# Optimization experiments

Measured on AMD Instinct MI355X. Metric: run time of the kernel, lower is better.

## Reference

```python
import jax, jax.numpy as jnp
import numpy as np

N_NODES = 100000

def _gcn_layer(h, src, dst, norm, W, b, n_nodes):
    # GCNConv: x @ W, then symmetric-normalized scatter-add over edges (incl. self-loops)
    h = h @ W                                  # [N, F_out]
    msg = h[src] * norm[:, None]               # [E_tot, F_out]
    out = jax.ops.segment_sum(msg, dst, num_segments=n_nodes)
    return out + b


def setup_inputs() -> dict:
    key = jax.random.key(0)
    k1, k2, k3, k4 = jax.random.split(key, 4)
    N, E, F_in, H, C = N_NODES, 3200000, 128, 16, 16
    x = jax.random.normal(k1, (N, F_in), dtype=jnp.float32)
    edge_index = jax.random.randint(k2, (2, E), 0, N, dtype=jnp.int64)
    W1 = jax.random.normal(k3, (F_in, H), dtype=jnp.float32) * (1.0 / np.sqrt(F_in))
    b1 = jnp.zeros((H,), dtype=jnp.float32)
    W2 = jax.random.normal(k4, (H, C), dtype=jnp.float32) * (1.0 / np.sqrt(H))
    b2 = jnp.zeros((C,), dtype=jnp.float32)
    return {"x": x, "edge_index": edge_index, "W1": W1, "b1": b1, "W2": W2, "b2": b2}


def reference(x, edge_index, W1, b1, W2, b2):
    N = x.shape[0]
    loops = jnp.arange(N, dtype=edge_index.dtype)
    src = jnp.concatenate([edge_index[0], loops])  # messages flow src -> dst (PyG convention)
    dst = jnp.concatenate([edge_index[1], loops])
    # symmetric normalization: deg^{-1/2}[src] * deg^{-1/2}[dst], deg counted on dst w/ self-loops
    deg = jnp.zeros((N,), dtype=x.dtype).at[dst].add(1.0)
    dinv = jax.lax.rsqrt(jnp.where(deg > 0, deg, 1.0))
    norm = dinv[src] * dinv[dst]                   # [E_tot]

    h = _gcn_layer(x, src, dst, norm, W1, b1, N)
    h = jax.nn.relu(h)
    # F.dropout(training=self.training): eval mode -> identity (deterministic reference)
    h = _gcn_layer(h, src, dst, norm, W2, b2, N)
    return jax.nn.log_softmax(h, axis=1)
```

## Files before the change

### kernel.cpp

```cpp
#include <hip/hip_runtime.h>
#include <hip/hip_bf16.h>
#include <math.h>


#define F_IN 128
#define H 16
#define NPB 128
#define MAX_NB 800
#define NBLK 256
#define BINT 1024
#define SMAX 4864
#define PFD 6

typedef __hip_bfloat16 bf16;

__device__ __forceinline__ float bflo(unsigned v) { return __uint_as_float(v << 16); }
__device__ __forceinline__ float bfhi(unsigned v) { return __uint_as_float(v & 0xffff0000u); }

__device__ __forceinline__ int swz(int p) { return (p & 7) * 32 + (p >> 3); }

__global__ void bin1_kernel(const int* __restrict__ src, const int* __restrict__ dst,
                            int* __restrict__ gcursor, unsigned* __restrict__ packed,
                            int E, int NB) {
    __shared__ int h[MAX_NB];
    __shared__ int pos[MAX_NB];
    int b = swz(blockIdx.x);
    long long e0 = (long long)E * b / NBLK;
    long long e1 = (long long)E * (b + 1) / NBLK;
    for (int i = threadIdx.x; i < NB; i += BINT) h[i] = 0;
    __syncthreads();
    for (long long e = e0 + threadIdx.x; e < e1; e += BINT)
        atomicAdd(&h[dst[e] >> 7], 1);
    __syncthreads();
    for (int i = threadIdx.x; i < NB; i += BINT) {
        int c = h[i];
        pos[i] = (c > 0) ? atomicAdd(&gcursor[i], c) : 0;
    }
    __syncthreads();
    for (long long e = e0 + threadIdx.x; e < e1; e += BINT) {
        int d = dst[e];
        int bk = d >> 7;
        int loc = atomicAdd(&pos[bk], 1);
        if (loc < SMAX)
            packed[(size_t)bk * SMAX + loc] = (unsigned)src[e] | ((unsigned)(d & 127) << 17);
    }
}

__global__ void bucketscan_kernel(const int* __restrict__ gcursor, int* __restrict__ base, int NB) {
    __shared__ int s[1024];
    int t = threadIdx.x;
    int v = 0;
    if (t < NB) { v = gcursor[t]; if (v > SMAX) v = SMAX; }
    s[t] = v;
    __syncthreads();
    for (int off = 1; off < 1024; off <<= 1) {
        int w = (t >= off) ? s[t - off] : 0;
        __syncthreads();
        s[t] += w;
        __syncthreads();
    }
    if (t < NB) base[t] = s[t] - v;
    if (t == NB - 1) base[NB] = s[t];
}

__global__ void sortcsr_kernel(const unsigned* __restrict__ packed, const int* __restrict__ gcursor,
                               const int* __restrict__ base, unsigned* __restrict__ sorted,
                               int* __restrict__ rowptr, float* __restrict__ dinv, int N) {
    __shared__ unsigned ssort[SMAX];
    __shared__ int cnt[NPB], offs[NPB], cur[NPB];
    int b = blockIdx.x;
    int rp = b * SMAX;
    int len = gcursor[b];
    if (len > SMAX) len = SMAX;
    int e0 = base[b];
    int T = blockDim.x;

    for (int i = threadIdx.x; i < NPB; i += T) cnt[i] = 0;
    __syncthreads();
    for (int i = threadIdx.x; i < len; i += T)
        atomicAdd(&cnt[packed[rp + i] >> 17], 1);
    __syncthreads();
    if (threadIdx.x < NPB) offs[threadIdx.x] = cnt[threadIdx.x];
    __syncthreads();
    for (int off = 1; off < NPB; off <<= 1) {
        int v = 0;
        if (threadIdx.x < NPB && threadIdx.x >= off) v = offs[threadIdx.x - off];
        __syncthreads();
        if (threadIdx.x < NPB) offs[threadIdx.x] += v;
        __syncthreads();
    }
    if (threadIdx.x < NPB) {
        int ex = offs[threadIdx.x] - cnt[threadIdx.x];
        cur[threadIdx.x] = ex;
        int node = b * NPB + threadIdx.x;
        if (node < N) {
            rowptr[node] = e0 + ex;
            dinv[node] = rsqrtf(1.0f + (float)cnt[threadIdx.x]);
        }
    }
    __syncthreads();
    for (int i = threadIdx.x; i < len; i += T) {
        unsigned p = packed[rp + i];
        int pos = atomicAdd(&cur[p >> 17], 1);
        ssort[pos] = p;
    }
    __syncthreads();
    for (int i = threadIdx.x; i < len; i += T) sorted[e0 + i] = ssort[i];
    if (b == 0 && threadIdx.x == 0) rowptr[N] = base[gridDim.x];
}

#define XPAD 132
__global__ void xw1_kernel(const float* __restrict__ x, const float* __restrict__ W1,
                           const float* __restrict__ dinv, bf16* __restrict__ u, int n) {
    __shared__ float sW1[F_IN * H];
    __shared__ float sx[16 * XPAD];
    for (int t = threadIdx.x; t < F_IN * H; t += blockDim.x) sW1[t] = W1[t];

    int basei = blockIdx.x * 16;
    for (int idx = threadIdx.x; idx < 512; idx += 256) {
        int r = idx >> 5;
        int kk = (idx & 31) << 2;
        int row = basei + r;
        float4 v = make_float4(0.f, 0.f, 0.f, 0.f);
        if (row < n) v = *(const float4*)(x + (size_t)row * F_IN + kk);
        *(float4*)(sx + r * XPAD + kk) = v;
    }
    __syncthreads();

    int r = threadIdx.x >> 4;
    int j = threadIdx.x & 15;
    int row = basei + r;
    if (row >= n) return;

    const float* xr = sx + r * XPAD;
    float acc = 0.0f;
#pragma unroll 16
    for (int k = 0; k < F_IN; k++) acc += xr[k] * sW1[k * H + j];
    u[(size_t)row * H + j] = __float2bfloat16(dinv[row] * acc);
}

#define GATHER_TILE(UVPTR)                                                      \
    int lane = threadIdx.x & 63;                                                \
    int wave = threadIdx.x >> 6;                                                \
    int j2 = lane & 7, g = lane >> 3;                                           \
    int nodeBase = blockIdx.x * 64 + wave * 16;                                 \
    int r0c = 0, r1c = 0;                                                       \
    unsigned svc[PFD]; unsigned uvc[PFD];                                       \
    {   int node = nodeBase;                                                    \
        if (node < N) { r0c = rowptr[node]; r1c = rowptr[node + 1]; }           \
        _Pragma("unroll")                                                       \
        for (int m = 0; m < PFD; m++) {                                         \
            int k = r0c + g + 8 * m;                                            \
            if (k < r1c) svc[m] = sorted[k];                                    \
        }                                                                       \
        _Pragma("unroll")                                                       \
        for (int m = 0; m < PFD; m++) {                                         \
            int k = r0c + g + 8 * m;                                            \
            if (k < r1c) uvc[m] = UVPTR[(size_t)(svc[m] & 0x1FFFF) * 8 + j2];   \
        }                                                                       \
    }                                                                           \
    for (int t = 0; t < 16; t++) {                                              \
        int r0n = 0, r1n = 0;                                                   \
        unsigned svn[PFD];                                                      \
        if (t < 15) {                                                           \
            int nn = nodeBase + t + 1;                                          \
            if (nn < N) { r0n = rowptr[nn]; r1n = rowptr[nn + 1]; }             \
            _Pragma("unroll")                                                   \
            for (int m = 0; m < PFD; m++) {                                     \
                int k = r0n + g + 8 * m;                                        \
                if (k < r1n) svn[m] = sorted[k];                                \
            }                                                                   \
        }                                                                       \
        float ax = 0.f, ay = 0.f;                                               \
        _Pragma("unroll")                                                       \
        for (int m = 0; m < PFD; m++) {                                         \
            int k = r0c + g + 8 * m;                                            \
            if (k < r1c) { ax += bflo(uvc[m]); ay += bfhi(uvc[m]); }            \
        }                                                                       \
        for (int k = r0c + g + 8 * PFD; k < r1c; k += 8) {                      \
            unsigned va = UVPTR[(size_t)(sorted[k] & 0x1FFFF) * 8 + j2];        \
            ax += bflo(va); ay += bfhi(va);                                     \
        }                                                                       \
        ax += __shfl_xor(ax, 8);  ay += __shfl_xor(ay, 8);                      \
        ax += __shfl_xor(ax, 16); ay += __shfl_xor(ay, 16);                     \
        ax += __shfl_xor(ax, 32); ay += __shfl_xor(ay, 32);                     \
        if (g == 0) {                                                           \
            tile[(wave * 16 + t) * 16 + 2 * j2] = ax;                           \
            tile[(wave * 16 + t) * 16 + 2 * j2 + 1] = ay;                       \
        }                                                                       \
        if (t < 15) {                                                           \
            r0c = r0n; r1c = r1n;                                               \
            _Pragma("unroll")                                                   \
            for (int m = 0; m < PFD; m++) {                                     \
                int k = r0n + g + 8 * m;                                        \
                svc[m] = svn[m];                                                \
                if (k < r1n) uvc[m] = UVPTR[(size_t)(svn[m] & 0x1FFFF) * 8 + j2]; \
            }                                                                   \
        }                                                                       \
    }

__global__ void gatherfin1_kernel(const unsigned* __restrict__ sorted, const int* __restrict__ rowptr,
                                  const bf16* __restrict__ u, const float* __restrict__ dinv,
                                  const float* __restrict__ b1, const float* __restrict__ W2,
                                  bf16* __restrict__ u2, int N) {
    __shared__ float tile[64 * 16];
    __shared__ float sW2[256];
    __shared__ float sb1[16];
    sW2[threadIdx.x] = W2[threadIdx.x];
    if (threadIdx.x < 16) sb1[threadIdx.x] = b1[threadIdx.x];

    const unsigned* uvp = (const unsigned*)u;
    GATHER_TILE(uvp)
    __syncthreads();

    int jj = threadIdx.x & 15;
    for (int rr = 0; rr < 4; rr++) {
        int rl = (threadIdx.x >> 4) + rr * 16;
        int node = blockIdx.x * 64 + rl;
        float h = 0.f, di = 0.f;
        if (node < N) {
            di = dinv[node];
            h = di * (tile[rl * 16 + jj] + __bfloat162float(u[(size_t)node * H + jj])) + sb1[jj];
            h = fmaxf(h, 0.f);
        }
        float acc2 = 0.f;
#pragma unroll
        for (int kk = 0; kk < 16; kk++) {
            float hk = __shfl(h, kk, 16);
            acc2 += hk * sW2[kk * 16 + jj];
        }
        if (node < N) u2[(size_t)node * H + jj] = __float2bfloat16(di * acc2);
    }
}

__global__ void gatherfin2_kernel(const unsigned* __restrict__ sorted, const int* __restrict__ rowptr,
                                  const bf16* __restrict__ u2, const float* __restrict__ dinv,
                                  const float* __restrict__ b2, float* __restrict__ out, int N) {
    __shared__ float tile[64 * 16];
    __shared__ float sb2[16];
    if (threadIdx.x < 16) sb2[threadIdx.x] = b2[threadIdx.x];

    const unsigned* uvp = (const unsigned*)u2;
    GATHER_TILE(uvp)
    __syncthreads();

    int jj = threadIdx.x & 15;
    for (int rr = 0; rr < 4; rr++) {
        int rl = (threadIdx.x >> 4) + rr * 16;
        int node = blockIdx.x * 64 + rl;
        if (node >= N) continue;
        float di = dinv[node];
        float v = di * (tile[rl * 16 + jj] + __bfloat162float(u2[(size_t)node * H + jj])) + sb2[jj];

        float m = v;
#pragma unroll
        for (int off = 8; off >= 1; off >>= 1) m = fmaxf(m, __shfl_xor(m, off, 16));
        float ex = __expf(v - m);
        float s = ex;
#pragma unroll
        for (int off = 8; off >= 1; off >>= 1) s += __shfl_xor(s, off, 16);

        out[(size_t)node * H + jj] = v - m - __logf(s);
    }
}

extern "C" void kernel_launch(void* const* d_in, const int* in_sizes, int n_in,
                              void* d_out, int out_size, void* d_ws, size_t ws_size,
                              hipStream_t stream) {
    const float* x = (const float*)d_in[0];
    const int* edge_index = (const int*)d_in[1];
    const float* W1 = (const float*)d_in[2];
    const float* b1 = (const float*)d_in[3];
    const float* W2 = (const float*)d_in[4];
    const float* b2 = (const float*)d_in[5];
    float* out = (float*)d_out;

    const int N = in_sizes[0] / F_IN;
    const int E = in_sizes[1] / 2;
    const int* src = edge_index;
    const int* dst = edge_index + E;
    const int NB = (N + NPB - 1) / NPB;

    float* dinv = (float*)d_ws;
    bf16* u = (bf16*)(dinv + N);
    bf16* u2 = (bf16*)((unsigned*)u + (size_t)N * H / 2);
    unsigned* packed = (unsigned*)((unsigned*)u2 + (size_t)N * H / 2);
    unsigned* sorted = packed + (size_t)NB * SMAX;
    int* rowptr = (int*)(sorted + E);
    int* gcursor = rowptr + N + 1;
    int* base = gcursor + NB;

    hipMemsetAsync(gcursor, 0, NB * sizeof(int), stream);

    bin1_kernel<<<NBLK, BINT, 0, stream>>>(src, dst, gcursor, packed, E, NB);
    bucketscan_kernel<<<1, 1024, 0, stream>>>(gcursor, base, NB);
    sortcsr_kernel<<<NB, 512, 0, stream>>>(packed, gcursor, base, sorted, rowptr, dinv, N);

    xw1_kernel<<<(N + 15) / 16, 256, 0, stream>>>(x, W1, dinv, u, N);
    gatherfin1_kernel<<<(N + 63) / 64, 256, 0, stream>>>(sorted, rowptr, u, dinv, b1, W2, u2, N);
    gatherfin2_kernel<<<(N + 63) / 64, 256, 0, stream>>>(sorted, rowptr, u2, dinv, b2, out, N);
}
```

Baseline: 251.8 us.

## Replace global-atomic binning with per-block local bucket sort and gather

The first binning pass now sorts each block's edge chunk by destination bucket in shared memory and writes it contiguously, recording per-block bucket counts and offsets, in place of reserving space through global atomics and scattering 4-byte writes across buckets. The scan kernel sums the per-block counts, and the CSR sort kernel gathers each bucket's segments from all 256 source blocks into shared memory before the local node sort. This removes the global atomics and the memset, and turns scattered writes into coalesced ones. In exchange the scan does a serial 256-step loop per bucket, the sort kernel reads many short segments, and each block needs a 12800-entry shared buffer, which assumes a chunk never exceeds 12500 edges.

New measurement: 283.3 us. 1.13x slower.

```diff
diff --git a/kernel.cpp b/kernel.cpp
--- a/kernel.cpp
+++ b/kernel.cpp
@@ -9,6 +9,7 @@
 #define MAX_NB 800
 #define NBLK 256
 #define BINT 1024
+#define SBUF_MAX 12800
 #define SMAX 4864
 #define PFD 6
 
@@ -17,96 +18,139 @@
 __device__ __forceinline__ float bflo(unsigned v) { return __uint_as_float(v << 16); }
 __device__ __forceinline__ float bfhi(unsigned v) { return __uint_as_float(v & 0xffff0000u); }
 
-__device__ __forceinline__ int swz(int p) { return (p & 7) * 32 + (p >> 3); }
-
-__global__ void bin1_kernel(const int* __restrict__ src, const int* __restrict__ dst,
-                            int* __restrict__ gcursor, unsigned* __restrict__ packed,
-                            int E, int NB) {
-    __shared__ int h[MAX_NB];
-    __shared__ int pos[MAX_NB];
-    int b = swz(blockIdx.x);
+__global__ void binsort_kernel(const int* __restrict__ src, const int* __restrict__ dst,
+                               unsigned* __restrict__ packed, int* __restrict__ loff_t,
+                               int* __restrict__ cnt_t, int E, int NB) {
+    __shared__ int hist[MAX_NB];
+    __shared__ int cur[MAX_NB];
+    __shared__ int scan[1024];
+    __shared__ unsigned sbuf[SBUF_MAX];
+    int b = blockIdx.x;
     long long e0 = (long long)E * b / NBLK;
     long long e1 = (long long)E * (b + 1) / NBLK;
-    for (int i = threadIdx.x; i < NB; i += BINT) h[i] = 0;
-    __syncthreads();
-    for (long long e = e0 + threadIdx.x; e < e1; e += BINT)
-        atomicAdd(&h[dst[e] >> 7], 1);
-    __syncthreads();
-    for (int i = threadIdx.x; i < NB; i += BINT) {
-        int c = h[i];
-        pos[i] = (c > 0) ? atomicAdd(&gcursor[i], c) : 0;
-    }
-    __syncthreads();
-    for (long long e = e0 + threadIdx.x; e < e1; e += BINT) {
-        int d = dst[e];
+    int len = (int)(e1 - e0);
+    int t = threadIdx.x;
+
+    for (int i = t; i < NB; i += BINT) hist[i] = 0;
+    __syncthreads();
+    for (int i = t; i < len; i += BINT) atomicAdd(&hist[dst[e0 + i] >> 7], 1);
+    __syncthreads();
+    scan[t] = (t < NB) ? hist[t] : 0;
+    __syncthreads();
+    for (int off = 1; off < 1024; off <<= 1) {
+        int v = (t >= off) ? scan[t - off] : 0;
+        __syncthreads();
+        scan[t] += v;
+        __syncthreads();
+    }
+    if (t < NB) {
+        int ex = scan[t] - hist[t];
+        cur[t] = ex;
+        loff_t[b * MAX_NB + t] = ex;
+        cnt_t[b * MAX_NB + t] = hist[t];
+    }
+    __syncthreads();
+    for (int i = t; i < len; i += BINT) {
+        int d = dst[e0 + i];
         int bk = d >> 7;
-        int loc = atomicAdd(&pos[bk], 1);
-        if (loc < SMAX)
-            packed[(size_t)bk * SMAX + loc] = (unsigned)src[e] | ((unsigned)(d & 127) << 17);
-    }
-}
-
-__global__ void bucketscan_kernel(const int* __restrict__ gcursor, int* __restrict__ base, int NB) {
+        int p = atomicAdd(&cur[bk], 1);
+        sbuf[p] = (unsigned)src[e0 + i] | ((unsigned)(d & 127) << 17);
+    }
+    __syncthreads();
+    for (int i = t; i < len; i += BINT) packed[e0 + i] = sbuf[i];
+}
+
+__global__ void bucketscan_kernel(const int* __restrict__ cnt_t, int* __restrict__ base, int NB) {
     __shared__ int s[1024];
     int t = threadIdx.x;
-    int v = 0;
-    if (t < NB) { v = gcursor[t]; if (v > SMAX) v = SMAX; }
-    s[t] = v;
+    int tot = 0;
+    if (t < NB)
+        for (int blk = 0; blk < NBLK; blk++) tot += cnt_t[blk * MAX_NB + t];
+    if (tot > SMAX) tot = SMAX;
+    s[t] = (t < NB) ? tot : 0;
     __syncthreads();
     for (int off = 1; off < 1024; off <<= 1) {
-        int w = (t >= off) ? s[t - off] : 0;
-        __syncthreads();
-        s[t] += w;
-        __syncthreads();
-    }
-    if (t < NB) base[t] = s[t] - v;
+        int v = (t >= off) ? s[t - off] : 0;
+        __syncthreads();
+        s[t] += v;
+        __syncthreads();
+    }
+    if (t < NB) base[t] = s[t] - tot;
     if (t == NB - 1) base[NB] = s[t];
 }
 
-__global__ void sortcsr_kernel(const unsigned* __restrict__ packed, const int* __restrict__ gcursor,
-                               const int* __restrict__ base, unsigned* __restrict__ sorted,
-                               int* __restrict__ rowptr, float* __restrict__ dinv, int N) {
+__global__ void sortcsr_kernel(const unsigned* __restrict__ packed, const int* __restrict__ loff_t,
+                               const int* __restrict__ cnt_t, const int* __restrict__ base,
+                               unsigned* __restrict__ sorted, int* __restrict__ rowptr,
+                               float* __restrict__ dinv, int N, int E, int NB) {
+    __shared__ unsigned raw[SMAX];
     __shared__ unsigned ssort[SMAX];
+    __shared__ int c[NBLK], doff[NBLK];
     __shared__ int cnt[NPB], offs[NPB], cur[NPB];
+    __shared__ int slen;
     int b = blockIdx.x;
-    int rp = b * SMAX;
-    int len = gcursor[b];
+    int T = blockDim.x;
+    int t = threadIdx.x;
+
+    if (t < NBLK) { c[t] = cnt_t[t * MAX_NB + b]; doff[t] = c[t]; }
+    __syncthreads();
+    for (int off = 1; off < NBLK; off <<= 1) {
+        int v = 0;
+        if (t < NBLK && t >= off) v = doff[t - off];
+        __syncthreads();
+        if (t < NBLK) doff[t] += v;
+        __syncthreads();
+    }
+    if (t == NBLK - 1) slen = doff[t];
+    __syncthreads();
+    int len = slen;
     if (len > SMAX) len = SMAX;
-    int e0 = base[b];
-    int T = blockDim.x;
-
-    for (int i = threadIdx.x; i < NPB; i += T) cnt[i] = 0;
-    __syncthreads();
-    for (int i = threadIdx.x; i < len; i += T)
-        atomicAdd(&cnt[packed[rp + i] >> 17], 1);
-    __syncthreads();
-    if (threadIdx.x < NPB) offs[threadIdx.x] = cnt[threadIdx.x];
+
+    int wv = t >> 6, ln = t & 63;
+    for (int q = wv; q < NBLK; q += 8) {
+        int cq = c[q];
+        int dq = doff[q] - cq;
+        long long s0 = (long long)E * q / NBLK;
+        int so = (int)s0 + loff_t[q * MAX_NB + b];
+        for (int i = ln; i < cq; i += 64) {
+            int dp = dq + i;
+            if (dp < SMAX) raw[dp] = packed[so + i];
+        }
+    }
+    __syncthreads();
+
+    for (int i = t; i < NPB; i += T) cnt[i] = 0;
+    __syncthreads();
+    for (int i = t; i < len; i += T) atomicAdd(&cnt[raw[i] >> 17], 1);
+    __syncthreads();
+    if (t < NPB) offs[t] = cnt[t];
     __syncthreads();
     for (int off = 1; off < NPB; off <<= 1) {
         int v = 0;
-        if (threadIdx.x < NPB && threadIdx.x >= off) v = offs[threadIdx.x - off];
-        __syncthreads();
-        if (threadIdx.x < NPB) offs[threadIdx.x] += v;
-        __syncthreads();
-    }
-    if (threadIdx.x < NPB) {
-        int ex = offs[threadIdx.x] - cnt[threadIdx.x];
-        cur[threadIdx.x] = ex;
-        int node = b * NPB + threadIdx.x;
+        if (t < NPB && t >= off) v = offs[t - off];
+        __syncthreads();
+        if (t < NPB) offs[t] += v;
+        __syncthreads();
+    }
+    int e0 = base[b];
+    if (t < NPB) {
+        int ex = offs[t] - cnt[t];
+        cur[t] = ex;
+        int node = b * NPB + t;
         if (node < N) {
             rowptr[node] = e0 + ex;
-            dinv[node] = rsqrtf(1.0f + (float)cnt[threadIdx.x]);
+            dinv[node] = rsqrtf(1.0f + (float)cnt[t]);
         }
     }
     __syncthreads();
-    for (int i = threadIdx.x; i < len; i += T) {
-        unsigned p = packed[rp + i];
+    for (int i = t; i < len; i += T) {
+        unsigned p = raw[i];
         int pos = atomicAdd(&cur[p >> 17], 1);
         ssort[pos] = p;
     }
     __syncthreads();
-    for (int i = threadIdx.x; i < len; i += T) sorted[e0 + i] = ssort[i];
-    if (b == 0 && threadIdx.x == 0) rowptr[N] = base[gridDim.x];
+    for (int i = t; i < len; i += T) sorted[e0 + i] = ssort[i];
+    if (b == 0 && t == 0) rowptr[N] = base[NB];
 }
 
 #define XPAD 132
@@ -285,16 +329,15 @@
     bf16* u = (bf16*)(dinv + N);
     bf16* u2 = (bf16*)((unsigned*)u + (size_t)N * H / 2);
     unsigned* packed = (unsigned*)((unsigned*)u2 + (size_t)N * H / 2);
-    unsigned* sorted = packed + (size_t)NB * SMAX;
+    unsigned* sorted = packed + E;
     int* rowptr = (int*)(sorted + E);
-    int* gcursor = rowptr + N + 1;
-    int* base = gcursor + NB;
-
-    hipMemsetAsync(gcursor, 0, NB * sizeof(int), stream);
-
-    bin1_kernel<<<NBLK, BINT, 0, stream>>>(src, dst, gcursor, packed, E, NB);
-    bucketscan_kernel<<<1, 1024, 0, stream>>>(gcursor, base, NB);
-    sortcsr_kernel<<<NB, 512, 0, stream>>>(packed, gcursor, base, sorted, rowptr, dinv, N);
+    int* loff_t = rowptr + N + 1;
+    int* cnt_t = loff_t + (size_t)NBLK * MAX_NB;
+    int* base = cnt_t + (size_t)NBLK * MAX_NB;
+
+    binsort_kernel<<<NBLK, BINT, 0, stream>>>(src, dst, packed, loff_t, cnt_t, E, NB);
+    bucketscan_kernel<<<1, 1024, 0, stream>>>(cnt_t, base, NB);
+    sortcsr_kernel<<<NB, 512, 0, stream>>>(packed, loff_t, cnt_t, base, sorted, rowptr, dinv, N, E, NB);
 
     xw1_kernel<<<(N + 15) / 16, 256, 0, stream>>>(x, W1, dinv, u, N);
     gatherfin1_kernel<<<(N + 63) / 64, 256, 0, stream>>>(sorted, rowptr, u, dinv, b1, W2, u2, N);
```
